# Kernel tuning notes

Hardware: AMD Instinct MI355X
Metric: run time of the kernel (lower is better)

Reference implementation:

```python
import jax, jax.numpy as jnp
import numpy as np

N = 100000      # num_nodes
R = 8           # num_relations
D = 128         # hidden_dim
E = 600000      # num_edges
P = 100000      # num query pairs
PH = 128        # pair_hidden_dim


def _xavier(key, shape):
    fan_in, fan_out = shape[-2], shape[-1]
    limit = float(np.sqrt(6.0 / (fan_in + fan_out)))
    return jax.random.uniform(key, shape, jnp.float32, -limit, limit)


def setup_inputs() -> dict:
    key = jax.random.key(0)
    ks = jax.random.split(key, 16)
    edge_index = jax.random.randint(ks[0], (2, E), 0, N)
    edge_type = jax.random.randint(ks[1], (E,), 0, R)
    drug_index = jax.random.randint(ks[2], (P,), 0, N)
    disease_index = jax.random.randint(ks[3], (P,), 0, N)
    emb = _xavier(ks[4], (N, D))
    rw1 = _xavier(ks[5], (R, D, D))
    sl1 = _xavier(ks[6], (D, D))
    b1 = jnp.zeros((D,), jnp.float32)
    rw2 = _xavier(ks[7], (R, D, D))
    sl2 = _xavier(ks[8], (D, D))
    b2 = jnp.zeros((D,), jnp.float32)
    pw1 = _xavier(ks[9], (3 * D, PH))
    pb1 = jnp.zeros((PH,), jnp.float32)
    pw2 = _xavier(ks[10], (PH, 1))
    pb2 = jnp.zeros((1,), jnp.float32)
    return {
        "edge_index": edge_index, "edge_type": edge_type,
        "drug_index": drug_index, "disease_index": disease_index,
        "emb": emb, "rw1": rw1, "sl1": sl1, "b1": b1,
        "rw2": rw2, "sl2": sl2, "b2": b2,
        "pw1": pw1, "pb1": pb1, "pw2": pw2, "pb2": pb2,
    }


def _rgcn_layer(x, rel_w, self_w, bias, src, dst, etype):
    # Transform all node features once per relation: [R, N, D]
    xW = jnp.einsum('nd,rde->rne', x, rel_w)
    # Per-relation in-degree of dst (matches torch bincount-per-relation, clamp_min(1))
    seg_key = etype * N + dst                                  # [E]
    deg = jax.ops.segment_sum(jnp.ones((src.shape[0],), x.dtype), seg_key,
                              num_segments=R * N)
    deg = jnp.maximum(deg, 1.0)
    msg = xW[etype, src] / deg[seg_key][:, None]               # [E, D]
    agg = jax.ops.segment_sum(msg, dst, num_segments=N)        # [N, D]
    return x @ self_w + agg + bias


def reference(edge_index, edge_type, drug_index, disease_index,
              emb, rw1, sl1, b1, rw2, sl2, b2, pw1, pb1, pw2, pb2):
    src, dst = edge_index[0], edge_index[1]
    # encode (eval mode: dropout is identity)
    x = _rgcn_layer(emb, rw1, sl1, b1, src, dst, edge_type)
    x = jax.nn.relu(x)
    x = _rgcn_layer(x, rw2, sl2, b2, src, dst, edge_type)
    # score_pairs
    dh = x[drug_index]
    sh = x[disease_index]
    feat = jnp.concatenate((dh, sh, dh * sh), axis=-1)         # [P, 3D]
    h = jax.nn.relu(feat @ pw1 + pb1)
    logits = (h @ pw2 + pb2)[:, 0]                             # [P]
    return logits
```

## Files before the change

### kernel.cpp

```cpp
#include <hip/hip_runtime.h>

#define D 128
#define RMAX 16

typedef short s16x8 __attribute__((ext_vector_type(8)));
typedef float f32x4 __attribute__((ext_vector_type(4)));

__device__ inline unsigned short f2b(float f) {
    unsigned u = __builtin_bit_cast(unsigned, f);
    unsigned r = (u + 0x7FFFu + ((u >> 16) & 1u)) >> 16;
    return (unsigned short)r;
}
__device__ inline float b2f(unsigned short h) {
    unsigned u = ((unsigned)h) << 16;
    return __builtin_bit_cast(float, u);
}


__global__ void k_count(const int* __restrict__ etype, const int* __restrict__ dst,
                        int E, int N, int R, int* __restrict__ deg, int* __restrict__ counts) {
    __shared__ int lh[RMAX];
    if (threadIdx.x < RMAX) lh[threadIdx.x] = 0;
    __syncthreads();
    int e = blockIdx.x * blockDim.x + threadIdx.x;
    if (e < E) {
        int r = etype[e];
        atomicAdd(&deg[r * N + dst[e]], 1);
        atomicAdd(&lh[r], 1);
    }
    __syncthreads();
    if (threadIdx.x < R && lh[threadIdx.x])
        atomicAdd(&counts[threadIdx.x], lh[threadIdx.x]);
}

__global__ void k_offsets(const int* __restrict__ counts, int* __restrict__ po,
                          int* __restrict__ cursors, int R, int N) {
    if (threadIdx.x == 0 && blockIdx.x == 0) {
        int acc = 0;
        for (int r = 0; r < R; ++r) {
            po[r] = acc;
            cursors[r] = acc;
            acc += ((counts[r] + 127) / 128) * 128;
        }
        po[R] = acc;
        acc += ((N + 127) / 128) * 128;
        po[R + 1] = acc;
    }
}

__global__ void k_scatter(const int* __restrict__ etype, int E, int R,
                          int* __restrict__ cursors, int* __restrict__ perm) {
    __shared__ int lh[RMAX];
    __shared__ int lbase[RMAX];
    __shared__ int lcur[RMAX];
    if (threadIdx.x < RMAX) lh[threadIdx.x] = 0;
    __syncthreads();
    int e = blockIdx.x * blockDim.x + threadIdx.x;
    int r = -1;
    if (e < E) { r = etype[e]; atomicAdd(&lh[r], 1); }
    __syncthreads();
    if (threadIdx.x < R) {
        lbase[threadIdx.x] = lh[threadIdx.x] ? atomicAdd(&cursors[threadIdx.x], lh[threadIdx.x]) : 0;
        lcur[threadIdx.x] = 0;
    }
    __syncthreads();
    if (e < E) {
        int pos = lbase[r] + atomicAdd(&lcur[r], 1);
        perm[pos] = e;
    }
}

__global__ void k_selfperm(const int* __restrict__ po, int R, int E, int N,
                           int* __restrict__ perm) {
    int n = blockIdx.x * 256 + threadIdx.x;
    if (n < N) perm[po[R] + n] = E + n;
}


__global__ void k_indeg(const int* __restrict__ deg, int* __restrict__ cnt, int N, int R) {
    int d = blockIdx.x * 256 + threadIdx.x;
    if (d < N) {
        int s = 1;
        for (int r = 0; r < R; ++r) s += deg[r * N + d];
        cnt[d] = s;
    }
}

__global__ void k_scan1(const int* __restrict__ cnt, int* __restrict__ tmp,
                        int* __restrict__ bsum, int N) {
    __shared__ int sd[256];
    int t = threadIdx.x;
    int base = blockIdx.x * 1024 + t * 4;
    int s[4];
    #pragma unroll
    for (int k = 0; k < 4; ++k) s[k] = (base + k < N) ? cnt[base + k] : 0;
    int tsum = s[0] + s[1] + s[2] + s[3];
    sd[t] = tsum;
    __syncthreads();
    for (int off = 1; off < 256; off <<= 1) {
        int v = (t >= off) ? sd[t - off] : 0;
        __syncthreads();
        sd[t] += v;
        __syncthreads();
    }
    int excl = sd[t] - tsum;
    int run = excl;
    #pragma unroll
    for (int k = 0; k < 4; ++k) {
        if (base + k < N) tmp[base + k] = run;
        run += s[k];
    }
    if (t == 255) bsum[blockIdx.x] = sd[255];
}

__global__ void k_scan2(const int* __restrict__ bsum, int* __restrict__ boff,
                        int nb, int* __restrict__ rowstart, int N, int total) {
    __shared__ int sd[256];
    int t = threadIdx.x;
    int v = (t < nb) ? bsum[t] : 0;
    sd[t] = v;
    __syncthreads();
    for (int off = 1; off < 256; off <<= 1) {
        int w = (t >= off) ? sd[t - off] : 0;
        __syncthreads();
        sd[t] += w;
        __syncthreads();
    }
    if (t < nb) boff[t] = sd[t] - v;
    if (t == 0) rowstart[N] = total;
}

__global__ void k_scan3(const int* __restrict__ tmp, const int* __restrict__ boff,
                        int* __restrict__ rowstart, int N) {
    int i = blockIdx.x * 256 + threadIdx.x;
    if (i < N) rowstart[i] = tmp[i] + boff[i >> 10];
}

__global__ void k_dstpos(const int* __restrict__ dstA, const int* __restrict__ rowstart,
                         int* __restrict__ cur2, int* __restrict__ dstpos, int E, int N) {
    int t = blockIdx.x * 256 + threadIdx.x;
    if (t < E) {
        int d = dstA[t];
        int rank = atomicAdd(&cur2[d], 1);
        dstpos[t] = rowstart[d] + 1 + rank;
    } else if (t < E + N) {
        dstpos[t] = rowstart[t - E];
    }
}


__global__ void k_tobf16(const float* __restrict__ in, unsigned short* __restrict__ out, long n) {
    long i = ((long)blockIdx.x * 256 + threadIdx.x) * 4;
    if (i >= n) return;
    f32x4 v = *(const f32x4*)(in + i);
    unsigned u0 = (unsigned)f2b(v[0]) | ((unsigned)f2b(v[1]) << 16);
    unsigned u1 = (unsigned)f2b(v[2]) | ((unsigned)f2b(v[3]) << 16);
    uint2 t; t.x = u0; t.y = u1;
    *(uint2*)(out + i) = t;
}

__global__ void k_transpose_b(const float* __restrict__ in, unsigned short* __restrict__ out,
                              int B, int K, int Ncol) {
    int idx = blockIdx.x * 256 + threadIdx.x;
    int per = K * Ncol;
    if (idx >= B * per) return;
    int b = idx / per, rem = idx - b * per;
    int n = rem / K, k = rem - n * K;
    out[idx] = f2b(in[(size_t)b * per + (size_t)k * Ncol + n]);
}


__global__ __launch_bounds__(256) void k_gemm_msg(
    const unsigned short* __restrict__ xb,
    const unsigned short* __restrict__ wAll,
    const int* __restrict__ perm,
    const int* __restrict__ srcA, const int* __restrict__ dstA,
    const int* __restrict__ deg, const int* __restrict__ dstpos,
    const int* __restrict__ po, int E, int N, int Rt,
    unsigned short* __restrict__ y)
{
    __shared__ unsigned char smB[32768];
    __shared__ int   ssrc[128];
    __shared__ float sscale[128];
    __shared__ int   sdp[128];
    int tid = threadIdx.x;
    int row0 = blockIdx.x * 128;
    if (row0 >= po[Rt]) return;
    int r = 0;
    while (row0 >= po[r + 1]) ++r;

    if (tid < 128) {
        int p = perm[row0 + tid];
        int sv = 0; float sc = 0.0f; int dp = -1;
        if (p >= 0) {
            dp = dstpos[p];
            if (p < E) { sv = srcA[p]; sc = 1.0f / (float)deg[r * N + dstA[p]]; }
            else       { sv = p - E;   sc = 1.0f; }
        }
        ssrc[tid] = sv; sscale[tid] = sc; sdp[tid] = dp;
    }
    {
        const int4* src = (const int4*)(wAll + (size_t)r * D * D);
        #pragma unroll
        for (int i = 0; i < 8; ++i) {
            int q = tid + i * 256;
            int n = q >> 4, c = q & 15;
            int4 v = src[q];
            *(int4*)(smB + n * 256 + ((c * 16) ^ ((n & 7) << 4))) = v;
        }
    }
    __syncthreads();

    int lane = tid & 63, wid = tid >> 6;
    int lo = lane & 15, hi = lane >> 4;
    int r0g = wid * 32 + lo, r1g = r0g + 16;
    const unsigned short* xrow0 = xb + (size_t)ssrc[r0g] * D;
    const unsigned short* xrow1 = xb + (size_t)ssrc[r1g] * D;

    f32x4 acc[2][8];
    #pragma unroll
    for (int a = 0; a < 2; ++a)
        #pragma unroll
        for (int b = 0; b < 8; ++b) acc[a][b] = (f32x4){0, 0, 0, 0};

    #pragma unroll
    for (int ks = 0; ks < 4; ++ks) {
        s16x8 a0 = *(const s16x8*)(xrow0 + ks * 32 + hi * 8);
        s16x8 a1 = *(const s16x8*)(xrow1 + ks * 32 + hi * 8);
        int kb = ks * 64 + hi * 16;
        #pragma unroll
        for (int n = 0; n < 8; ++n) {
            int cr = n * 16 + lo;
            s16x8 bf = *(const s16x8*)(smB + cr * 256 + (kb ^ ((cr & 7) << 4)));
            acc[0][n] = __builtin_amdgcn_mfma_f32_16x16x32_bf16(a0, bf, acc[0][n], 0, 0, 0);
            acc[1][n] = __builtin_amdgcn_mfma_f32_16x16x32_bf16(a1, bf, acc[1][n], 0, 0, 0);
        }
    }

    __syncthreads();
    #pragma unroll
    for (int m2 = 0; m2 < 2; ++m2) {
        int rbase = wid * 32 + m2 * 16 + hi * 4;
        #pragma unroll
        for (int reg = 0; reg < 4; ++reg) {
            int rl = rbase + reg;
            float s = sscale[rl];
            #pragma unroll
            for (int n = 0; n < 8; ++n) {
                int byteoff = rl * 256 + (((n * 32 + (lo >> 3) * 16) ^ ((rl & 7) << 4)) + (lo & 7) * 2);
                *(unsigned short*)(smB + byteoff) = f2b(acc[m2][n][reg] * s);
            }
        }
    }
    __syncthreads();
    {
        int m = tid >> 1, half = tid & 1;
        int dp = sdp[m];
        if (dp >= 0) {
            unsigned short* dst = y + (size_t)dp * D;
            #pragma unroll
            for (int i = 0; i < 8; ++i) {
                int c = half * 8 + i;
                int4 v = *(const int4*)(smB + m * 256 + ((c * 16) ^ ((m & 7) << 4)));
                *(int4*)(dst + c * 8) = v;
            }
        }
    }
}


template<bool RELU>
__global__ void k_reduce(const unsigned short* __restrict__ y,
                         const int* __restrict__ rowstart,
                         const float* __restrict__ bias,
                         unsigned short* __restrict__ out, int N)
{
    int tid = threadIdx.x;
    int dl = tid >> 6, cj = tid & 63;
    int dbase = blockIdx.x * 16 + dl * 4;
    float b0 = bias[cj * 2], b1 = bias[cj * 2 + 1];
    for (int i = 0; i < 4; ++i) {
        int d = dbase + i;
        if (d >= N) return;
        int s = rowstart[d], e = rowstart[d + 1];
        float a0 = b0, a1 = b1;
        for (int pos = s; pos < e; ++pos) {
            unsigned v = *(const unsigned*)(y + (size_t)pos * D + cj * 2);
            a0 += __builtin_bit_cast(float, (v & 0xFFFFu) << 16);
            a1 += __builtin_bit_cast(float, v & 0xFFFF0000u);
        }
        if (RELU) { a0 = fmaxf(a0, 0.0f); a1 = fmaxf(a1, 0.0f); }
        unsigned o = (unsigned)f2b(a0) | ((unsigned)f2b(a1) << 16);
        *(unsigned*)(out + (size_t)d * D + cj * 2) = o;
    }
}


__global__ __launch_bounds__(256) void k_score(
    const unsigned short* __restrict__ x2b,
    const int* __restrict__ drug, const int* __restrict__ dis,
    const unsigned short* __restrict__ pw1T,
    const float* __restrict__ pb1, const float* __restrict__ pw2,
    const float* __restrict__ pb2, float* __restrict__ outp, int P)
{
    __shared__ unsigned char smA[32768];
    __shared__ unsigned char smB[32768];
    __shared__ float pb1s[128];
    __shared__ float pw2s[128];
    int tid = threadIdx.x;
    long p0 = (long)blockIdx.x * 128;
    if (tid < 128) { pb1s[tid] = pb1[tid]; pw2s[tid] = pw2[tid]; }
    float pb2v = pb2[0];

    int lane = tid & 63, wid = tid >> 6;
    int lo = lane & 15, hi = lane >> 4;
    f32x4 acc[2][8];
    #pragma unroll
    for (int a = 0; a < 2; ++a)
        #pragma unroll
        for (int b = 0; b < 8; ++b) acc[a][b] = (f32x4){0, 0, 0, 0};

    for (int ch = 0; ch < 3; ++ch) {
        {
            const unsigned char* pbT = (const unsigned char*)pw1T;
            #pragma unroll
            for (int i = 0; i < 8; ++i) {
                int q = tid + i * 256;
                int n = q >> 4, c = q & 15;
                int4 v = *(const int4*)(pbT + (size_t)n * 768 + ch * 256 + c * 16);
                *(int4*)(smB + n * 256 + ((c * 16) ^ ((n & 7) << 4))) = v;
            }
        }
        {
            int m = tid >> 1, half = tid & 1;
            long p = p0 + m;
            int4 z = {0, 0, 0, 0};
            if (p < P) {
                const int4* da = (const int4*)(x2b + (size_t)drug[p] * D);
                const int4* db = (const int4*)(x2b + (size_t)dis[p] * D);
                for (int c = half * 8; c < half * 8 + 8; ++c) {
                    int4 v;
                    if (ch == 0) v = da[c];
                    else if (ch == 1) v = db[c];
                    else {
                        int4 va = da[c], vb = db[c];
                        const unsigned short* ap = (const unsigned short*)&va;
                        const unsigned short* bp = (const unsigned short*)&vb;
                        unsigned short o[8];
                        #pragma unroll
                        for (int j = 0; j < 8; ++j) o[j] = f2b(b2f(ap[j]) * b2f(bp[j]));
                        v = *(const int4*)o;
                    }
                    *(int4*)(smA + m * 256 + ((c * 16) ^ ((m & 7) << 4))) = v;
                }
            } else {
                for (int c = half * 8; c < half * 8 + 8; ++c)
                    *(int4*)(smA + m * 256 + ((c * 16) ^ ((m & 7) << 4))) = z;
            }
        }
        __syncthreads();

        #pragma unroll
        for (int ks = 0; ks < 4; ++ks) {
            int kb = ks * 64 + hi * 16;
            int r0 = wid * 32 + lo, r1 = r0 + 16;
            s16x8 a0 = *(const s16x8*)(smA + r0 * 256 + (kb ^ ((r0 & 7) << 4)));
            s16x8 a1 = *(const s16x8*)(smA + r1 * 256 + (kb ^ ((r1 & 7) << 4)));
            #pragma unroll
            for (int n = 0; n < 8; ++n) {
                int cr = n * 16 + lo;
                s16x8 bf = *(const s16x8*)(smB + cr * 256 + (kb ^ ((cr & 7) << 4)));
                acc[0][n] = __builtin_amdgcn_mfma_f32_16x16x32_bf16(a0, bf, acc[0][n], 0, 0, 0);
                acc[1][n] = __builtin_amdgcn_mfma_f32_16x16x32_bf16(a1, bf, acc[1][n], 0, 0, 0);
            }
        }
        __syncthreads();
    }

    #pragma unroll
    for (int m2 = 0; m2 < 2; ++m2)
        #pragma unroll
        for (int reg = 0; reg < 4; ++reg) {
            float s = 0.0f;
            #pragma unroll
            for (int n = 0; n < 8; ++n) {
                int col = n * 16 + lo;
                float v = acc[m2][n][reg] + pb1s[col];
                v = fmaxf(v, 0.0f);
                s = fmaf(v, pw2s[col], s);
            }
            s += __shfl_xor(s, 1, 64);
            s += __shfl_xor(s, 2, 64);
            s += __shfl_xor(s, 4, 64);
            s += __shfl_xor(s, 8, 64);
            long p = p0 + wid * 32 + m2 * 16 + hi * 4 + reg;
            if (lo == 0 && p < P) outp[p] = s + pb2v;
        }
}


extern "C" void kernel_launch(void* const* d_in, const int* in_sizes, int n_in,
                              void* d_out, int out_size, void* d_ws, size_t ws_size,
                              hipStream_t stream) {
    const int*   edge_index = (const int*)d_in[0];
    const int*   edge_type  = (const int*)d_in[1];
    const int*   drug       = (const int*)d_in[2];
    const int*   dis        = (const int*)d_in[3];
    const float* emb        = (const float*)d_in[4];
    const float* rw1        = (const float*)d_in[5];
    const float* sl1        = (const float*)d_in[6];
    const float* b1         = (const float*)d_in[7];
    const float* rw2        = (const float*)d_in[8];
    const float* sl2        = (const float*)d_in[9];
    const float* b2         = (const float*)d_in[10];
    const float* pw1        = (const float*)d_in[11];
    const float* pb1        = (const float*)d_in[12];
    const float* pw2        = (const float*)d_in[13];
    const float* pb2        = (const float*)d_in[14];

    const int E = in_sizes[1];
    const int P = in_sizes[2];
    const int N = in_sizes[4] / D;
    const int R = in_sizes[5] / (D * D);

    const int* srcA = edge_index;
    const int* dstA = edge_index + E;

    const int permN = E + ((N + 127) / 128) * 128 + (R + 1) * 128;

    char* ws = (char*)d_ws;
    unsigned short* embb = (unsigned short*)ws; ws += (size_t)N * D * 2;
    unsigned short* x1b  = (unsigned short*)ws; ws += (size_t)N * D * 2;
    unsigned short* y    = (unsigned short*)ws; ws += (size_t)(E + N) * D * 2;
    unsigned short* wAll1 = (unsigned short*)ws; ws += (size_t)(R + 1) * D * D * 2;
    unsigned short* wAll2 = (unsigned short*)ws; ws += (size_t)(R + 1) * D * D * 2;
    unsigned short* pw1T  = (unsigned short*)ws; ws += (size_t)3 * D * D * 2;
    int* deg     = (int*)ws; ws += (size_t)R * N * 4;
    int* perm    = (int*)ws; ws += (size_t)permN * 4;
    int* dstpos  = (int*)ws; ws += (size_t)(E + N) * 4;
    int* cnt     = (int*)ws; ws += (size_t)N * 4;
    int* tmp     = (int*)ws; ws += (size_t)N * 4;
    int* rowstart = (int*)ws; ws += (size_t)(N + 1) * 4;
    int* cur2    = (int*)ws; ws += (size_t)N * 4;
    int* bsum    = (int*)ws; ws += 256 * 4;
    int* boff    = (int*)ws; ws += 256 * 4;
    int* counts  = (int*)ws; ws += 256;
    int* po      = (int*)ws; ws += 256;
    int* cursors = (int*)ws; ws += 256;
    unsigned short* x2b = embb;

    hipMemsetAsync(deg, 0, (size_t)R * N * 4, stream);
    hipMemsetAsync(counts, 0, 256, stream);
    hipMemsetAsync(cur2, 0, (size_t)N * 4, stream);
    hipMemsetAsync(perm, 0xFF, (size_t)permN * 4, stream);

    k_count  <<<(E + 255) / 256, 256, 0, stream>>>(edge_type, dstA, E, N, R, deg, counts);
    k_offsets<<<1, 1, 0, stream>>>(counts, po, cursors, R, N);
    k_scatter<<<(E + 255) / 256, 256, 0, stream>>>(edge_type, E, R, cursors, perm);
    k_selfperm<<<(N + 255) / 256, 256, 0, stream>>>(po, R, E, N, perm);

    k_indeg<<<(N + 255) / 256, 256, 0, stream>>>(deg, cnt, N, R);
    int nb1 = (N + 1023) / 1024;
    k_scan1<<<nb1, 256, 0, stream>>>(cnt, tmp, bsum, N);
    k_scan2<<<1, 256, 0, stream>>>(bsum, boff, nb1, rowstart, N, E + N);
    k_scan3<<<(N + 255) / 256, 256, 0, stream>>>(tmp, boff, rowstart, N);
    k_dstpos<<<(E + N + 255) / 256, 256, 0, stream>>>(dstA, rowstart, cur2, dstpos, E, N);

    long nd = (long)N * D;
    k_tobf16<<<(int)((nd / 4 + 255) / 256), 256, 0, stream>>>(emb, embb, nd);
    k_transpose_b<<<(R * D * D + 255) / 256, 256, 0, stream>>>(rw1, wAll1, R, D, D);
    k_transpose_b<<<(D * D + 255) / 256, 256, 0, stream>>>(sl1, wAll1 + (size_t)R * D * D, 1, D, D);
    k_transpose_b<<<(R * D * D + 255) / 256, 256, 0, stream>>>(rw2, wAll2, R, D, D);
    k_transpose_b<<<(D * D + 255) / 256, 256, 0, stream>>>(sl2, wAll2 + (size_t)R * D * D, 1, D, D);
    k_transpose_b<<<(3 * D * D + 255) / 256, 256, 0, stream>>>(pw1, pw1T, 1, 3 * D, D);

    int gridM = (E + 127) / 128 + (N + 127) / 128 + R + 2;
    int gridR = (N + 15) / 16;

    k_gemm_msg<<<gridM, 256, 0, stream>>>(embb, wAll1, perm, srcA, dstA, deg, dstpos,
                                          po, E, N, R + 1, y);
    k_reduce<true><<<gridR, 256, 0, stream>>>(y, rowstart, b1, x1b, N);
    k_gemm_msg<<<gridM, 256, 0, stream>>>(x1b, wAll2, perm, srcA, dstA, deg, dstpos,
                                          po, E, N, R + 1, y);
    k_reduce<false><<<gridR, 256, 0, stream>>>(y, rowstart, b2, x2b, N);
    k_score<<<(P + 127) / 128, 256, 0, stream>>>(x2b, drug, dis, pw1T, pb1, pw2, pb2,
                                                 (float*)d_out, P);
}
```

Baseline: 513.8 us.

## Sort edges by source within relation, fuse prep kernels, widen reduce loads

Edges are now counting-sorted by (relation, source) instead of only by relation, so consecutive GEMM rows gather the same or nearby source rows for better cache reuse. The identity/self rows are derived from indices instead of a materialized perm, and the A-row gather loads are issued before the weight tile is staged into shared memory. Weight pre-swizzling moves into a single fused prep kernel that also converts embeddings, replacing several launches. The reduce kernel now loads 8 bf16 per thread with 16-byte vectors. The extra scan over R*N source bins and the added atomics cost some preprocessing time.

```diff
diff --git a/kernel.cpp b/kernel.cpp
--- a/kernel.cpp
+++ b/kernel.cpp
@@ -17,15 +17,18 @@
 }
 
 
-__global__ void k_count(const int* __restrict__ etype, const int* __restrict__ dst,
-                        int E, int N, int R, int* __restrict__ deg, int* __restrict__ counts) {
+__global__ void k_count2(const int* __restrict__ etype, const int* __restrict__ srcA,
+                         const int* __restrict__ dstA, int E, int N, int R,
+                         int* __restrict__ deg, int* __restrict__ srcCnt,
+                         int* __restrict__ counts) {
     __shared__ int lh[RMAX];
     if (threadIdx.x < RMAX) lh[threadIdx.x] = 0;
     __syncthreads();
     int e = blockIdx.x * blockDim.x + threadIdx.x;
     if (e < E) {
         int r = etype[e];
-        atomicAdd(&deg[r * N + dst[e]], 1);
+        atomicAdd(&deg[r * N + dstA[e]], 1);
+        atomicAdd(&srcCnt[r * N + srcA[e]], 1);
         atomicAdd(&lh[r], 1);
     }
     __syncthreads();
@@ -34,12 +37,11 @@
 }
 
 __global__ void k_offsets(const int* __restrict__ counts, int* __restrict__ po,
-                          int* __restrict__ cursors, int R, int N) {
+                          int R, int N) {
     if (threadIdx.x == 0 && blockIdx.x == 0) {
         int acc = 0;
         for (int r = 0; r < R; ++r) {
             po[r] = acc;
-            cursors[r] = acc;
             acc += ((counts[r] + 127) / 128) * 128;
         }
         po[R] = acc;
@@ -48,53 +50,17 @@
     }
 }
 
-__global__ void k_scatter(const int* __restrict__ etype, int E, int R,
-                          int* __restrict__ cursors, int* __restrict__ perm) {
-    __shared__ int lh[RMAX];
-    __shared__ int lbase[RMAX];
-    __shared__ int lcur[RMAX];
-    if (threadIdx.x < RMAX) lh[threadIdx.x] = 0;
-    __syncthreads();
-    int e = blockIdx.x * blockDim.x + threadIdx.x;
-    int r = -1;
-    if (e < E) { r = etype[e]; atomicAdd(&lh[r], 1); }
-    __syncthreads();
-    if (threadIdx.x < R) {
-        lbase[threadIdx.x] = lh[threadIdx.x] ? atomicAdd(&cursors[threadIdx.x], lh[threadIdx.x]) : 0;
-        lcur[threadIdx.x] = 0;
-    }
-    __syncthreads();
-    if (e < E) {
-        int pos = lbase[r] + atomicAdd(&lcur[r], 1);
-        perm[pos] = e;
-    }
-}
-
-__global__ void k_selfperm(const int* __restrict__ po, int R, int E, int N,
-                           int* __restrict__ perm) {
-    int n = blockIdx.x * 256 + threadIdx.x;
-    if (n < N) perm[po[R] + n] = E + n;
-}
-
-
-__global__ void k_indeg(const int* __restrict__ deg, int* __restrict__ cnt, int N, int R) {
-    int d = blockIdx.x * 256 + threadIdx.x;
-    if (d < N) {
-        int s = 1;
-        for (int r = 0; r < R; ++r) s += deg[r * N + d];
-        cnt[d] = s;
-    }
-}
-
-__global__ void k_scan1(const int* __restrict__ cnt, int* __restrict__ tmp,
-                        int* __restrict__ bsum, int N) {
+
+template<int VPT>
+__global__ void k_scan_blk(const int* __restrict__ in, int* __restrict__ tmp,
+                           int* __restrict__ bsum, int n) {
     __shared__ int sd[256];
     int t = threadIdx.x;
-    int base = blockIdx.x * 1024 + t * 4;
-    int s[4];
-    #pragma unroll
-    for (int k = 0; k < 4; ++k) s[k] = (base + k < N) ? cnt[base + k] : 0;
-    int tsum = s[0] + s[1] + s[2] + s[3];
+    long base = (long)blockIdx.x * (256 * VPT) + (long)t * VPT;
+    int s[VPT];
+    int tsum = 0;
+    #pragma unroll
+    for (int k = 0; k < VPT; ++k) { s[k] = (base + k < n) ? in[base + k] : 0; tsum += s[k]; }
     sd[t] = tsum;
     __syncthreads();
     for (int off = 1; off < 256; off <<= 1) {
@@ -103,18 +69,45 @@
         sd[t] += v;
         __syncthreads();
     }
-    int excl = sd[t] - tsum;
-    int run = excl;
+    int run = sd[t] - tsum;
+    #pragma unroll
+    for (int k = 0; k < VPT; ++k) { if (base + k < n) tmp[base + k] = run; run += s[k]; }
+    if (t == 255) bsum[blockIdx.x] = sd[255];
+}
+
+__global__ void k_scanD1(const int* __restrict__ deg, int* __restrict__ tmp,
+                         int* __restrict__ bsum, int N, int R) {
+    __shared__ int sd[256];
+    int t = threadIdx.x;
+    long base = (long)blockIdx.x * 1024 + (long)t * 4;
+    int s[4];
+    int tsum = 0;
     #pragma unroll
     for (int k = 0; k < 4; ++k) {
-        if (base + k < N) tmp[base + k] = run;
-        run += s[k];
-    }
+        int v = 0;
+        long d = base + k;
+        if (d < N) {
+            v = 1;
+            for (int r = 0; r < R; ++r) v += deg[(size_t)r * N + d];
+        }
+        s[k] = v; tsum += v;
+    }
+    sd[t] = tsum;
+    __syncthreads();
+    for (int off = 1; off < 256; off <<= 1) {
+        int v = (t >= off) ? sd[t - off] : 0;
+        __syncthreads();
+        sd[t] += v;
+        __syncthreads();
+    }
+    int run = sd[t] - tsum;
+    #pragma unroll
+    for (int k = 0; k < 4; ++k) { if (base + k < N) tmp[base + k] = run; run += s[k]; }
     if (t == 255) bsum[blockIdx.x] = sd[255];
 }
 
-__global__ void k_scan2(const int* __restrict__ bsum, int* __restrict__ boff,
-                        int nb, int* __restrict__ rowstart, int N, int total) {
+__global__ void k_scan2(const int* __restrict__ bsum, int* __restrict__ boff, int nb,
+                        int* __restrict__ tail, int tailval) {
     __shared__ int sd[256];
     int t = threadIdx.x;
     int v = (t < nb) ? bsum[t] : 0;
@@ -127,46 +120,83 @@
         __syncthreads();
     }
     if (t < nb) boff[t] = sd[t] - v;
-    if (t == 0) rowstart[N] = total;
+    if (t == 0 && tail) *tail = tailval;
 }
 
 __global__ void k_scan3(const int* __restrict__ tmp, const int* __restrict__ boff,
-                        int* __restrict__ rowstart, int N) {
+                        int* __restrict__ out, int n, int shift) {
     int i = blockIdx.x * 256 + threadIdx.x;
-    if (i < N) rowstart[i] = tmp[i] + boff[i >> 10];
+    if (i < n) out[i] = tmp[i] + boff[i >> shift];
+}
+
+
+__global__ void k_scatter2(const int* __restrict__ etype, const int* __restrict__ srcA,
+                           int E, int N, const int* __restrict__ srcOff,
+                           const int* __restrict__ po, int* __restrict__ srcCur,
+                           int* __restrict__ perm) {
+    int e = blockIdx.x * blockDim.x + threadIdx.x;
+    if (e < E) {
+        int r = etype[e];
+        int bin = r * N + srcA[e];
+        int rank = atomicAdd(&srcCur[bin], 1);
+        int pos = po[r] + (srcOff[bin] - srcOff[r * N]) + rank;
+        perm[pos] = e;
+    }
 }
 
 __global__ void k_dstpos(const int* __restrict__ dstA, const int* __restrict__ rowstart,
-                         int* __restrict__ cur2, int* __restrict__ dstpos, int E, int N) {
+                         int* __restrict__ cur2, int* __restrict__ dstpos, int E) {
     int t = blockIdx.x * 256 + threadIdx.x;
     if (t < E) {
         int d = dstA[t];
         int rank = atomicAdd(&cur2[d], 1);
         dstpos[t] = rowstart[d] + 1 + rank;
-    } else if (t < E + N) {
-        dstpos[t] = rowstart[t - E];
-    }
-}
-
-
-__global__ void k_tobf16(const float* __restrict__ in, unsigned short* __restrict__ out, long n) {
-    long i = ((long)blockIdx.x * 256 + threadIdx.x) * 4;
-    if (i >= n) return;
-    f32x4 v = *(const f32x4*)(in + i);
-    unsigned u0 = (unsigned)f2b(v[0]) | ((unsigned)f2b(v[1]) << 16);
-    unsigned u1 = (unsigned)f2b(v[2]) | ((unsigned)f2b(v[3]) << 16);
-    uint2 t; t.x = u0; t.y = u1;
-    *(uint2*)(out + i) = t;
-}
-
-__global__ void k_transpose_b(const float* __restrict__ in, unsigned short* __restrict__ out,
-                              int B, int K, int Ncol) {
-    int idx = blockIdx.x * 256 + threadIdx.x;
-    int per = K * Ncol;
-    if (idx >= B * per) return;
-    int b = idx / per, rem = idx - b * per;
-    int n = rem / K, k = rem - n * K;
-    out[idx] = f2b(in[(size_t)b * per + (size_t)k * Ncol + n]);
+    }
+}
+
+
+__global__ void k_prep(const float* __restrict__ emb,
+                       const float* __restrict__ rw1, const float* __restrict__ sl1,
+                       const float* __restrict__ rw2, const float* __restrict__ sl2,
+                       const float* __restrict__ pw1,
+                       unsigned short* __restrict__ embb,
+                       unsigned short* __restrict__ wAll1,
+                       unsigned short* __restrict__ wAll2,
+                       unsigned short* __restrict__ pw1T,
+                       int N, int R)
+{
+    long t = (long)blockIdx.x * 256 + threadIdx.x;
+    long u0 = (long)N * D / 4;
+    if (t < u0) {
+        long i = t * 4;
+        f32x4 v = *(const f32x4*)(emb + i);
+        unsigned a0 = (unsigned)f2b(v[0]) | ((unsigned)f2b(v[1]) << 16);
+        unsigned a1 = (unsigned)f2b(v[2]) | ((unsigned)f2b(v[3]) << 16);
+        uint2 o; o.x = a0; o.y = a1;
+        *(uint2*)(embb + i) = o;
+        return;
+    }
+    t -= u0;
+    long uW = (long)(R + 1) * D * D;
+    if (t < 2 * uW) {
+        const float* rw = (t < uW) ? rw1 : rw2;
+        const float* sl = (t < uW) ? sl1 : sl2;
+        unsigned short* o = (t < uW) ? wAll1 : wAll2;
+        long u = (t < uW) ? t : t - uW;
+        int r = (int)(u >> 14);
+        int nb = (int)(u & 16383);
+        int n = nb >> 7, kk = nb & 127;
+        int ke = kk ^ ((n & 7) << 3);
+        float v = (r < R) ? rw[((size_t)r * D + ke) * D + n] : sl[(size_t)ke * D + n];
+        o[u] = f2b(v);
+        return;
+    }
+    t -= 2 * uW;
+    if (t < 3 * D * D) {
+        int n = (int)(t / 384), ck = (int)(t - n * 384);
+        int ch = ck >> 7, kl = (ck & 127) ^ ((n & 7) << 3);
+        pw1T[t] = f2b(pw1[(size_t)(ch * 128 + kl) * 128 + n]);
+    }
 }
 
 
@@ -176,46 +206,67 @@
     const int* __restrict__ perm,
     const int* __restrict__ srcA, const int* __restrict__ dstA,
     const int* __restrict__ deg, const int* __restrict__ dstpos,
-    const int* __restrict__ po, int E, int N, int Rt,
+    const int* __restrict__ rowstart,
+    const int* __restrict__ po, const int* __restrict__ counts,
+    int E, int N, int R,
     unsigned short* __restrict__ y)
 {
     __shared__ unsigned char smB[32768];
-    __shared__ int   ssrc[128];
     __shared__ float sscale[128];
     __shared__ int   sdp[128];
     int tid = threadIdx.x;
     int row0 = blockIdx.x * 128;
-    if (row0 >= po[Rt]) return;
+    if (row0 >= po[R + 1]) return;
     int r = 0;
     while (row0 >= po[r + 1]) ++r;
+    int po_r = po[r];
+    int cnt_r = (r < R) ? counts[r] : N;
+
+    int lane = tid & 63, wid = tid >> 6;
+    int lo = lane & 15, hi = lane >> 4;
+
+    int r0g = wid * 32 + lo, r1g = r0g + 16;
+    int idx0 = row0 - po_r + r0g, idx1 = idx0 + 16;
+    int sv0 = 0, sv1 = 0;
+    if (r < R) {
+        if (idx0 < cnt_r) sv0 = srcA[perm[row0 + r0g]];
+        if (idx1 < cnt_r) sv1 = srcA[perm[row0 + r1g]];
+    } else {
+        if (idx0 < N) sv0 = idx0;
+        if (idx1 < N) sv1 = idx1;
+    }
+    const unsigned short* xrow0 = xb + (size_t)sv0 * D;
+    const unsigned short* xrow1 = xb + (size_t)sv1 * D;
+    s16x8 a0[4], a1[4];
+    #pragma unroll
+    for (int ks = 0; ks < 4; ++ks) {
+        a0[ks] = *(const s16x8*)(xrow0 + ks * 32 + hi * 8);
+        a1[ks] = *(const s16x8*)(xrow1 + ks * 32 + hi * 8);
+    }
 
     if (tid < 128) {
-        int p = perm[row0 + tid];
-        int sv = 0; float sc = 0.0f; int dp = -1;
-        if (p >= 0) {
-            dp = dstpos[p];
-            if (p < E) { sv = srcA[p]; sc = 1.0f / (float)deg[r * N + dstA[p]]; }
-            else       { sv = p - E;   sc = 1.0f; }
-        }
-        ssrc[tid] = sv; sscale[tid] = sc; sdp[tid] = dp;
-    }
+        int idx = row0 - po_r + tid;
+        float sc = 0.0f; int dp = -1;
+        if (r < R) {
+            if (idx < cnt_r) {
+                int p = perm[row0 + tid];
+                dp = dstpos[p];
+                sc = 1.0f / (float)deg[(size_t)r * N + dstA[p]];
+            }
+        } else if (idx < N) {
+            dp = rowstart[idx];
+            sc = 1.0f;
+        }
+        sscale[tid] = sc; sdp[tid] = dp;
+    }
+
     {
         const int4* src = (const int4*)(wAll + (size_t)r * D * D);
-        #pragma unroll
-        for (int i = 0; i < 8; ++i) {
-            int q = tid + i * 256;
-            int n = q >> 4, c = q & 15;
-            int4 v = src[q];
-            *(int4*)(smB + n * 256 + ((c * 16) ^ ((n & 7) << 4))) = v;
-        }
-    }
-    __syncthreads();
-
-    int lane = tid & 63, wid = tid >> 6;
-    int lo = lane & 15, hi = lane >> 4;
-    int r0g = wid * 32 + lo, r1g = r0g + 16;
-    const unsigned short* xrow0 = xb + (size_t)ssrc[r0g] * D;
-    const unsigned short* xrow1 = xb + (size_t)ssrc[r1g] * D;
+        int4* dstl = (int4*)smB;
+        #pragma unroll
+        for (int i = 0; i < 8; ++i) dstl[tid + i * 256] = src[tid + i * 256];
+    }
+    __syncthreads();
 
     f32x4 acc[2][8];
     #pragma unroll
@@ -225,15 +276,13 @@
 
     #pragma unroll
     for (int ks = 0; ks < 4; ++ks) {
-        s16x8 a0 = *(const s16x8*)(xrow0 + ks * 32 + hi * 8);
-        s16x8 a1 = *(const s16x8*)(xrow1 + ks * 32 + hi * 8);
         int kb = ks * 64 + hi * 16;
         #pragma unroll
         for (int n = 0; n < 8; ++n) {
             int cr = n * 16 + lo;
             s16x8 bf = *(const s16x8*)(smB + cr * 256 + (kb ^ ((cr & 7) << 4)));
-            acc[0][n] = __builtin_amdgcn_mfma_f32_16x16x32_bf16(a0, bf, acc[0][n], 0, 0, 0);
-            acc[1][n] = __builtin_amdgcn_mfma_f32_16x16x32_bf16(a1, bf, acc[1][n], 0, 0, 0);
+            acc[0][n] = __builtin_amdgcn_mfma_f32_16x16x32_bf16(a0[ks], bf, acc[0][n], 0, 0, 0);
+            acc[1][n] = __builtin_amdgcn_mfma_f32_16x16x32_bf16(a1[ks], bf, acc[1][n], 0, 0, 0);
         }
     }
 
@@ -276,22 +325,31 @@
                          unsigned short* __restrict__ out, int N)
 {
     int tid = threadIdx.x;
-    int dl = tid >> 6, cj = tid & 63;
-    int dbase = blockIdx.x * 16 + dl * 4;
-    float b0 = bias[cj * 2], b1 = bias[cj * 2 + 1];
+    int dl = tid >> 4, cj = tid & 15;
+    float b[8];
+    *(f32x4*)(b)     = *(const f32x4*)(bias + cj * 8);
+    *(f32x4*)(b + 4) = *(const f32x4*)(bias + cj * 8 + 4);
+    int dbase = blockIdx.x * 64 + dl * 4;
     for (int i = 0; i < 4; ++i) {
         int d = dbase + i;
         if (d >= N) return;
         int s = rowstart[d], e = rowstart[d + 1];
-        float a0 = b0, a1 = b1;
+        float a[8];
+        #pragma unroll
+        for (int j = 0; j < 8; ++j) a[j] = b[j];
         for (int pos = s; pos < e; ++pos) {
-            unsigned v = *(const unsigned*)(y + (size_t)pos * D + cj * 2);
-            a0 += __builtin_bit_cast(float, (v & 0xFFFFu) << 16);
-            a1 += __builtin_bit_cast(float, v & 0xFFFF0000u);
-        }
-        if (RELU) { a0 = fmaxf(a0, 0.0f); a1 = fmaxf(a1, 0.0f); }
-        unsigned o = (unsigned)f2b(a0) | ((unsigned)f2b(a1) << 16);
-        *(unsigned*)(out + (size_t)d * D + cj * 2) = o;
+            int4 v = *(const int4*)(y + (size_t)pos * D + cj * 8);
+            const unsigned short* hp = (const unsigned short*)&v;
+            #pragma unroll
+            for (int j = 0; j < 8; ++j) a[j] += b2f(hp[j]);
+        }
+        unsigned short o[8];
+        #pragma unroll
+        for (int j = 0; j < 8; ++j) {
+            float v = RELU ? fmaxf(a[j], 0.0f) : a[j];
+            o[j] = f2b(v);
+        }
+        *(int4*)(out + (size_t)d * D + cj * 8) = *(const int4*)o;
     }
 }
 
@@ -322,13 +380,13 @@
 
     for (int ch = 0; ch < 3; ++ch) {
         {
-            const unsigned char* pbT = (const unsigned char*)pw1T;
+            const int4* src = (const int4*)pw1T;
+            int4* dstl = (int4*)smB;
             #pragma unroll
             for (int i = 0; i < 8; ++i) {
                 int q = tid + i * 256;
                 int n = q >> 4, c = q & 15;
-                int4 v = *(const int4*)(pbT + (size_t)n * 768 + ch * 256 + c * 16);
-                *(int4*)(smB + n * 256 + ((c * 16) ^ ((n & 7) << 4))) = v;
+                dstl[q] = src[n * 48 + ch * 16 + c];
             }
         }
         {
@@ -426,8 +484,6 @@
     const int* srcA = edge_index;
     const int* dstA = edge_index + E;
 
-    const int permN = E + ((N + 127) / 128) * 128 + (R + 1) * 128;
-
     char* ws = (char*)d_ws;
     unsigned short* embb = (unsigned short*)ws; ws += (size_t)N * D * 2;
     unsigned short* x1b  = (unsigned short*)ws; ws += (size_t)N * D * 2;
@@ -436,52 +492,56 @@
     unsigned short* wAll2 = (unsigned short*)ws; ws += (size_t)(R + 1) * D * D * 2;
     unsigned short* pw1T  = (unsigned short*)ws; ws += (size_t)3 * D * D * 2;
     int* deg     = (int*)ws; ws += (size_t)R * N * 4;
-    int* perm    = (int*)ws; ws += (size_t)permN * 4;
-    int* dstpos  = (int*)ws; ws += (size_t)(E + N) * 4;
-    int* cnt     = (int*)ws; ws += (size_t)N * 4;
-    int* tmp     = (int*)ws; ws += (size_t)N * 4;
+    int* srcCnt  = (int*)ws; ws += (size_t)R * N * 4;
+    int* srcCur  = (int*)ws; ws += (size_t)R * N * 4;
+    int* cur2    = (int*)ws; ws += (size_t)N * 4;
+    int* counts  = (int*)ws; ws += 256;
+    size_t zbytes = (size_t)(3 * R * N + N + 64) * 4;
+    int* perm    = (int*)ws; ws += (size_t)(E + 128 * (R + 1)) * 4;
+    int* dstpos  = (int*)ws; ws += (size_t)E * 4;
+    int* srcOff  = (int*)ws; ws += (size_t)R * N * 4;
+    int* dtmp    = (int*)ws; ws += (size_t)N * 4;
     int* rowstart = (int*)ws; ws += (size_t)(N + 1) * 4;
-    int* cur2    = (int*)ws; ws += (size_t)N * 4;
-    int* bsum    = (int*)ws; ws += 256 * 4;
-    int* boff    = (int*)ws; ws += 256 * 4;
-    int* counts  = (int*)ws; ws += 256;
+    int* bsumS   = (int*)ws; ws += 256 * 4;
+    int* boffS   = (int*)ws; ws += 256 * 4;
+    int* bsumD   = (int*)ws; ws += 256 * 4;
+    int* boffD   = (int*)ws; ws += 256 * 4;
     int* po      = (int*)ws; ws += 256;
-    int* cursors = (int*)ws; ws += 256;
     unsigned short* x2b = embb;
 
-    hipMemsetAsync(deg, 0, (size_t)R * N * 4, stream);
-    hipMemsetAsync(counts, 0, 256, stream);
-    hipMemsetAsync(cur2, 0, (size_t)N * 4, stream);
-    hipMemsetAsync(perm, 0xFF, (size_t)permN * 4, stream);
-
-    k_count  <<<(E + 255) / 256, 256, 0, stream>>>(edge_type, dstA, E, N, R, deg, counts);
-    k_offsets<<<1, 1, 0, stream>>>(counts, po, cursors, R, N);
-    k_scatter<<<(E + 255) / 256, 256, 0, stream>>>(edge_type, E, R, cursors, perm);
-    k_selfperm<<<(N + 255) / 256, 256, 0, stream>>>(po, R, E, N, perm);
-
-    k_indeg<<<(N + 255) / 256, 256, 0, stream>>>(deg, cnt, N, R);
-    int nb1 = (N + 1023) / 1024;
-    k_scan1<<<nb1, 256, 0, stream>>>(cnt, tmp, bsum, N);
-    k_scan2<<<1, 256, 0, stream>>>(bsum, boff, nb1, rowstart, N, E + N);
-    k_scan3<<<(N + 255) / 256, 256, 0, stream>>>(tmp, boff, rowstart, N);
-    k_dstpos<<<(E + N + 255) / 256, 256, 0, stream>>>(dstA, rowstart, cur2, dstpos, E, N);
-
-    long nd = (long)N * D;
-    k_tobf16<<<(int)((nd / 4 + 255) / 256), 256, 0, stream>>>(emb, embb, nd);
-    k_transpose_b<<<(R * D * D + 255) / 256, 256, 0, stream>>>(rw1, wAll1, R, D, D);
-    k_transpose_b<<<(D * D + 255) / 256, 256, 0, stream>>>(sl1, wAll1 + (size_t)R * D * D, 1, D, D);
-    k_transpose_b<<<(R * D * D + 255) / 256, 256, 0, stream>>>(rw2, wAll2, R, D, D);
-    k_transpose_b<<<(D * D + 255) / 256, 256, 0, stream>>>(sl2, wAll2 + (size_t)R * D * D, 1, D, D);
-    k_transpose_b<<<(3 * D * D + 255) / 256, 256, 0, stream>>>(pw1, pw1T, 1, 3 * D, D);
+    hipMemsetAsync(deg, 0, zbytes, stream);
+
+    long u0 = (long)N * D / 4;
+    long uW = (long)(R + 1) * D * D;
+    long utot = u0 + 2 * uW + 3 * D * D;
+    k_prep<<<(int)((utot + 255) / 256), 256, 0, stream>>>(emb, rw1, sl1, rw2, sl2, pw1,
+                                                          embb, wAll1, wAll2, pw1T, N, R);
+
+    k_count2<<<(E + 255) / 256, 256, 0, stream>>>(edge_type, srcA, dstA, E, N, R,
+                                                  deg, srcCnt, counts);
+    k_offsets<<<1, 1, 0, stream>>>(counts, po, R, N);
+
+    int nbS = (R * N + 4095) / 4096;
+    k_scan_blk<16><<<nbS, 256, 0, stream>>>(srcCnt, srcOff, bsumS, R * N);
+    k_scan2<<<1, 256, 0, stream>>>(bsumS, boffS, nbS, nullptr, 0);
+    k_scan3<<<(R * N + 255) / 256, 256, 0, stream>>>(srcOff, boffS, srcOff, R * N, 12);
+    k_scatter2<<<(E + 255) / 256, 256, 0, stream>>>(edge_type, srcA, E, N, srcOff, po,
+                                                    srcCur, perm);
+
+    int nbD = (N + 1023) / 1024;
+    k_scanD1<<<nbD, 256, 0, stream>>>(deg, dtmp, bsumD, N, R);
+    k_scan2<<<1, 256, 0, stream>>>(bsumD, boffD, nbD, rowstart + N, E + N);
+    k_scan3<<<(N + 255) / 256, 256, 0, stream>>>(dtmp, boffD, rowstart, N, 10);
+    k_dstpos<<<(E + 255) / 256, 256, 0, stream>>>(dstA, rowstart, cur2, dstpos, E);
 
     int gridM = (E + 127) / 128 + (N + 127) / 128 + R + 2;
-    int gridR = (N + 15) / 16;
+    int gridR = (N + 63) / 64;
 
     k_gemm_msg<<<gridM, 256, 0, stream>>>(embb, wAll1, perm, srcA, dstA, deg, dstpos,
-                                          po, E, N, R + 1, y);
+                                          rowstart, po, counts, E, N, R, y);
     k_reduce<true><<<gridR, 256, 0, stream>>>(y, rowstart, b1, x1b, N);
     k_gemm_msg<<<gridM, 256, 0, stream>>>(x1b, wAll2, perm, srcA, dstA, deg, dstpos,
-                                          po, E, N, R + 1, y);
+                                          rowstart, po, counts, E, N, R, y);
     k_reduce<false><<<gridR, 256, 0, stream>>>(y, rowstart, b2, x2b, N);
     k_score<<<(P + 127) / 128, 256, 0, stream>>>(x2b, drug, dis, pw1T, pb1, pw2, pb2,
                                                  (float*)d_out, P);
```

Measured after the change: 578.6 us. 12.6% more time.
